# Performance work log

Measured on AMD Instinct MI355X. Metric: run time of the kernel, lower is better.

The kernel has to match this reference:

```python
import jax, jax.numpy as jnp
import numpy as np

WORD_DEPTH, K, K2, L, FL, J = 128, 128, 128, 64, 3, 2


def conv1d(x, w, b):
    # x: [B, C, T], w: [O, I, k], VALID padding (matches nn.Conv1d default)
    y = jax.lax.conv_general_dilated(x, w, (1,), 'VALID',
                                     dimension_numbers=('NCH', 'OIH', 'NCH'))
    return y + b[None, :, None]


def encode(x, w1, b1, w2, b2, ws, bs):
    # x: [B, T, D] -> semantic vector [B, L]
    h = jnp.tanh(conv1d(x.transpose(0, 2, 1), w1, b1))   # [B, K, T-2]
    h = jnp.tanh(conv1d(h, w2, b2))                      # [B, K2, T-4]
    h = h.max(axis=2)                                    # kmax pooling, k=1
    return jnp.tanh(h @ ws.T + bs)                       # [B, L]


def setup_inputs() -> dict:
    key = jax.random.key(0)
    ks = jax.random.split(key, 20)
    B, T = 64, 2048
    s = 0.05
    return {
        'q':    jax.random.normal(ks[0], (B, T, WORD_DEPTH), jnp.float32),
        'pos':  jax.random.normal(ks[1], (B, T, WORD_DEPTH), jnp.float32),
        'negs': jax.random.normal(ks[2], (J, B, T, WORD_DEPTH), jnp.float32),
        'qw1': jax.random.normal(ks[3], (K, WORD_DEPTH, FL), jnp.float32) * s,
        'qb1': jnp.zeros((K,), jnp.float32),
        'qw2': jax.random.normal(ks[4], (K2, K, FL), jnp.float32) * s,
        'qb2': jnp.zeros((K2,), jnp.float32),
        'qsw': jax.random.normal(ks[5], (L, K2), jnp.float32) * s,
        'qsb': jnp.zeros((L,), jnp.float32),
        'dw1': jax.random.normal(ks[6], (K, WORD_DEPTH, FL), jnp.float32) * s,
        'db1': jnp.zeros((K,), jnp.float32),
        'dw2': jax.random.normal(ks[7], (K2, K, FL), jnp.float32) * s,
        'db2': jnp.zeros((K2,), jnp.float32),
        'dsw': jax.random.normal(ks[8], (L, K2), jnp.float32) * s,
        'dsb': jnp.zeros((L,), jnp.float32),
        'gw':  jnp.asarray(1.0, jnp.float32),   # learn_gamma Conv1d(1,1,1) weight
        'gb':  jnp.asarray(0.0, jnp.float32),   # learn_gamma bias
    }


def reference(q, pos, negs, qw1, qb1, qw2, qb2, qsw, qsb,
              dw1, db1, dw2, db2, dsw, dsb, gw, gb):
    Jn, B, T, D = negs.shape
    q_s = encode(q, qw1, qb1, qw2, qb2, qsw, qsb)                  # [B, L]
    pos_s = encode(pos, dw1, db1, dw2, db2, dsw, dsb)              # [B, L]
    neg_s = encode(negs.reshape(Jn * B, T, D),
                   dw1, db1, dw2, db2, dsw, dsb).reshape(Jn, B, L)
    pos_dot = jnp.einsum('bl,bl->b', q_s, pos_s)                   # [B]
    neg_dot = jnp.einsum('bl,jbl->bj', q_s, neg_s)                 # [B, J]
    dots = jnp.concatenate([pos_dot[:, None], neg_dot], axis=1)   # [B, J+1]
    with_gamma = gw * dots + gb                                    # conv1x1
    return jax.nn.softmax(with_gamma, axis=1)                      # [B, J+1]
```

## Files before the change

kernel.cpp:

```cpp
#include <hip/hip_runtime.h>
#include <stdint.h>


typedef __bf16 bf16x8 __attribute__((ext_vector_type(8)));
typedef __bf16 bf16x4 __attribute__((ext_vector_type(4)));
typedef float f32x16 __attribute__((ext_vector_type(16)));
typedef unsigned short u16x8 __attribute__((ext_vector_type(8)));

__device__ __forceinline__ unsigned short f2bf(float f) {
  unsigned u = __builtin_bit_cast(unsigned, f);
  u = u + 0x7FFFu + ((u >> 16) & 1u);
  return (unsigned short)(u >> 16);
}

__device__ __forceinline__ float fast_tanh(float x) {
  x = fminf(10.0f, fmaxf(-10.0f, x));
  float t = __builtin_amdgcn_exp2f(x * -2.8853900817779268f);
  return (1.0f - t) * __builtin_amdgcn_rcpf(1.0f + t);
}

__global__ void prep_kernel(const float* __restrict__ qw1, const float* __restrict__ qw2,
                            const float* __restrict__ dw1, const float* __restrict__ dw2,
                            unsigned short* __restrict__ W1f, unsigned short* __restrict__ W2f) {
  int gid = blockIdx.x * 256 + threadIdx.x;
  int which = gid >= 98304;
  int e = which ? gid - 98304 : gid;
  int br = e / 49152; int r = e % 49152;
  int f = r / 16384; int r2 = r & 16383;
  int kk = r2 >> 11; int row = (r2 >> 4) & 127; int hi = (r2 >> 3) & 1; int j = r2 & 7;
  int c = kk * 16 + hi * 8 + j;
  const float* src = which ? (br ? dw2 : qw2) : (br ? dw1 : qw1);
  (which ? W2f : W1f)[e] = f2bf(src[row * 384 + c * 3 + f]);
}

#define XS0    0
#define H1S0   32768
#define B1_OFF 64512
#define LDS_TOTAL 65024
#define YS 60
#define NWIN 18

__global__ __launch_bounds__(512) void cdssm_main(
    const float* __restrict__ q, const float* __restrict__ pos, const float* __restrict__ negs,
    const unsigned short* __restrict__ W1f, const unsigned short* __restrict__ W2f,
    const float* __restrict__ qb1, const float* __restrict__ db1,
    float* __restrict__ hpart) {
  extern __shared__ char lds[];
  const int tid = threadIdx.x;
  const int bid = blockIdx.x;
  const int seq = bid >> 1;
  const int half = bid & 1;
  const int branch = (seq < 64) ? 0 : 1;
  const float* xptr = (seq < 64) ? (q + (size_t)seq * 2048 * 128)
                    : (seq < 128) ? (pos + (size_t)(seq - 64) * 2048 * 128)
                                  : (negs + (size_t)(seq - 128) * 2048 * 128);
  const float* b1g = branch ? db1 : qb1;
  const int lo = half * 1022;
  const int hi = lo + 1022;

  if (tid < 128) ((float*)(lds + B1_OFF))[tid] = b1g[tid];

  const int lane = tid & 63;
  const int w = tid >> 6;
  const int lrow = lane & 31;
  const int hi5 = lane >> 5;
  const int role = w >> 2;
  const int kt = w & 3;
  const int hi16 = hi5 * 16;

  const unsigned short* wfb = (role ? W2f : W1f) + (size_t)branch * 49152
                              + (kt * 32 + lrow) * 16 + hi5 * 8;

  bf16x8 ap[16];
#pragma unroll
  for (int f = 0; f < 2; ++f)
#pragma unroll
    for (int kk = 0; kk < 8; ++kk)
      ap[f * 8 + kk] = __builtin_bit_cast(bf16x8,
          *(const u16x8*)(wfb + f * 16384 + kk * 2048));

  float vmax[16];
#pragma unroll
  for (int r = 0; r < 16; ++r) vmax[r] = -1e30f;

  const int slot_s = tid >> 4;
  const int d0_s = (tid & 15) * 8;

#pragma unroll
  for (int u = 0; u < 2; ++u) {
    int sl = slot_s + u * 32;
    int t = lo + sl; if (t > 2047) t = 2047;
    const float* src = xptr + ((size_t)t * 128 + d0_s);
    float4 v0 = *(const float4*)src;
    float4 v1 = *(const float4*)(src + 4);
    bf16x8 o;
    o[0] = (__bf16)v0.x; o[1] = (__bf16)v0.y; o[2] = (__bf16)v0.z; o[3] = (__bf16)v0.w;
    o[4] = (__bf16)v1.x; o[5] = (__bf16)v1.y; o[6] = (__bf16)v1.z; o[7] = (__bf16)v1.w;
    *(bf16x8*)(lds + XS0 + sl * 256 + ((d0_s * 2) ^ ((sl & 15) << 4))) = o;
  }
  __syncthreads();

  for (int i = 0; i <= NWIN; ++i) {
    float4 va[4];
    const bool doStage = (i < NWIN - 1);
    if (doStage) {
      const int tb = lo + (i + 1) * YS;
#pragma unroll
      for (int u = 0; u < 2; ++u) {
        int t = tb + slot_s + u * 32; if (t > 2047) t = 2047;
        const float* src = xptr + ((size_t)t * 128 + d0_s);
        va[2 * u]     = *(const float4*)src;
        va[2 * u + 1] = *(const float4*)(src + 4);
      }
    }

    if (role == 0) {
      if (i < NWIN) {
        const int xb = XS0 + (i & 1) * 16384;
        f32x16 acc0, acc1;
#pragma unroll
        for (int r = 0; r < 16; ++r) { acc0[r] = 0.f; acc1[r] = 0.f; }
#pragma unroll
        for (int f = 0; f < 2; ++f) {
          int sv0 = lrow + f;
          int sv1 = 32 + lrow + f; if (sv1 > 63) sv1 = 63;
          int b0 = xb + sv0 * 256, z0 = (sv0 & 15) << 4;
          int b1 = xb + sv1 * 256, z1 = (sv1 & 15) << 4;
#pragma unroll
          for (int kk = 0; kk < 8; ++kk) {
            int ko = kk * 32 + hi16;
            bf16x8 bv0 = __builtin_bit_cast(bf16x8,
                *(const u16x8*)(lds + b0 + (ko ^ z0)));
            acc0 = __builtin_amdgcn_mfma_f32_32x32x16_bf16(ap[f * 8 + kk], bv0, acc0, 0, 0, 0);
            bf16x8 bv1 = __builtin_bit_cast(bf16x8,
                *(const u16x8*)(lds + b1 + (ko ^ z1)));
            acc1 = __builtin_amdgcn_mfma_f32_32x32x16_bf16(ap[f * 8 + kk], bv1, acc1, 0, 0, 0);
          }
        }
        {
          int sv0 = lrow + 2;
          int sv1 = 32 + lrow + 2; if (sv1 > 63) sv1 = 63;
          int b0 = xb + sv0 * 256, z0 = (sv0 & 15) << 4;
          int b1 = xb + sv1 * 256, z1 = (sv1 & 15) << 4;
#pragma unroll
          for (int kk = 0; kk < 8; ++kk) {
            bf16x8 av = __builtin_bit_cast(bf16x8,
                *(const u16x8*)(wfb + 2 * 16384 + kk * 2048));
            int ko = kk * 32 + hi16;
            bf16x8 bv0 = __builtin_bit_cast(bf16x8,
                *(const u16x8*)(lds + b0 + (ko ^ z0)));
            acc0 = __builtin_amdgcn_mfma_f32_32x32x16_bf16(av, bv0, acc0, 0, 0, 0);
            bf16x8 bv1 = __builtin_bit_cast(bf16x8,
                *(const u16x8*)(lds + b1 + (ko ^ z1)));
            acc1 = __builtin_amdgcn_mfma_f32_32x32x16_bf16(av, bv1, acc1, 0, 0, 0);
          }
        }
        const int hb = H1S0 + (i & 1) * 15872;
#pragma unroll
        for (int p = 0; p < 2; ++p) {
          const f32x16 acc = p ? acc1 : acc0;
          int s = p * 32 + lrow;
          if (s < 62) {
            int wb2 = hb + s * 256;
            int wz = (s & 15) << 4;
#pragma unroll
            for (int qd = 0; qd < 4; ++qd) {
              int k0 = kt * 32 + qd * 8 + hi5 * 4;
              float4 bq = *(const float4*)(lds + B1_OFF + k0 * 4);
              bf16x4 hv;
              hv[0] = (__bf16)fast_tanh(acc[qd * 4 + 0] + bq.x);
              hv[1] = (__bf16)fast_tanh(acc[qd * 4 + 1] + bq.y);
              hv[2] = (__bf16)fast_tanh(acc[qd * 4 + 2] + bq.z);
              hv[3] = (__bf16)fast_tanh(acc[qd * 4 + 3] + bq.w);
              *(bf16x4*)(lds + wb2 + ((k0 * 2) ^ wz)) = hv;
            }
          }
        }
      }
    } else {
      if (i >= 1) {
        const int hb = H1S0 + ((i & 1) ^ 1) * 15872;
        f32x16 acc0, acc1;
#pragma unroll
        for (int r = 0; r < 16; ++r) { acc0[r] = 0.f; acc1[r] = 0.f; }
#pragma unroll
        for (int f = 0; f < 2; ++f) {
          int sv0 = lrow + f;
          int sv1 = 32 + lrow + f; if (sv1 > 61) sv1 = 61;
          int b0 = hb + sv0 * 256, z0 = (sv0 & 15) << 4;
          int b1 = hb + sv1 * 256, z1 = (sv1 & 15) << 4;
#pragma unroll
          for (int kk = 0; kk < 8; ++kk) {
            int ko = kk * 32 + hi16;
            bf16x8 bv0 = __builtin_bit_cast(bf16x8,
                *(const u16x8*)(lds + b0 + (ko ^ z0)));
            acc0 = __builtin_amdgcn_mfma_f32_32x32x16_bf16(ap[f * 8 + kk], bv0, acc0, 0, 0, 0);
            bf16x8 bv1 = __builtin_bit_cast(bf16x8,
                *(const u16x8*)(lds + b1 + (ko ^ z1)));
            acc1 = __builtin_amdgcn_mfma_f32_32x32x16_bf16(ap[f * 8 + kk], bv1, acc1, 0, 0, 0);
          }
        }
        {
          int sv0 = lrow + 2;
          int sv1 = 32 + lrow + 2; if (sv1 > 61) sv1 = 61;
          int b0 = hb + sv0 * 256, z0 = (sv0 & 15) << 4;
          int b1 = hb + sv1 * 256, z1 = (sv1 & 15) << 4;
#pragma unroll
          for (int kk = 0; kk < 8; ++kk) {
            bf16x8 av = __builtin_bit_cast(bf16x8,
                *(const u16x8*)(wfb + 2 * 16384 + kk * 2048));
            int ko = kk * 32 + hi16;
            bf16x8 bv0 = __builtin_bit_cast(bf16x8,
                *(const u16x8*)(lds + b0 + (ko ^ z0)));
            acc0 = __builtin_amdgcn_mfma_f32_32x32x16_bf16(av, bv0, acc0, 0, 0, 0);
            bf16x8 bv1 = __builtin_bit_cast(bf16x8,
                *(const u16x8*)(lds + b1 + (ko ^ z1)));
            acc1 = __builtin_amdgcn_mfma_f32_32x32x16_bf16(av, bv1, acc1, 0, 0, 0);
          }
        }
        const int base = lo + (i - 1) * YS;
        const bool valid0 = (base + lrow < hi);
        const int s2b = 32 + lrow;
        const bool valid1 = (s2b < YS) && (base + s2b < hi);
#pragma unroll
        for (int r = 0; r < 16; ++r) {
          float v0 = valid0 ? acc0[r] : -1e30f;
          float v1 = valid1 ? acc1[r] : -1e30f;
          vmax[r] = fmaxf(vmax[r], fmaxf(v0, v1));
        }
      }
    }

    if (doStage) {
      const int xbn = XS0 + ((i + 1) & 1) * 16384;
#pragma unroll
      for (int u = 0; u < 2; ++u) {
        int sl = slot_s + u * 32;
        const float* f0 = (const float*)&va[2 * u];
        bf16x8 o;
#pragma unroll
        for (int j = 0; j < 8; ++j) o[j] = (__bf16)f0[j];
        *(bf16x8*)(lds + xbn + sl * 256 + ((d0_s * 2) ^ ((sl & 15) << 4))) = o;
      }
    }
    __syncthreads();
  }

  if (role == 1) {
#pragma unroll
    for (int r = 0; r < 16; ++r) {
      float v = vmax[r];
      v = fmaxf(v, __shfl_xor(v, 1, 64));
      v = fmaxf(v, __shfl_xor(v, 2, 64));
      v = fmaxf(v, __shfl_xor(v, 4, 64));
      v = fmaxf(v, __shfl_xor(v, 8, 64));
      v = fmaxf(v, __shfl_xor(v, 16, 64));
      vmax[r] = v;
    }
  }
  float* hbuf = (float*)(lds + XS0);
  if (role == 1 && lrow == 0) {
#pragma unroll
    for (int r = 0; r < 16; ++r) {
      int rl = (r & 3) + 8 * (r >> 2) + 4 * hi5;
      hbuf[kt * 32 + rl] = vmax[r];
    }
  }
  __syncthreads();
  if (tid < 128) hpart[(size_t)bid * 128 + tid] = hbuf[tid];
}

__global__ void k2_proj(const float* __restrict__ hpart,
                        const float* __restrict__ qsw, const float* __restrict__ qsb,
                        const float* __restrict__ dsw, const float* __restrict__ dsb,
                        const float* __restrict__ qb2, const float* __restrict__ db2,
                        float* __restrict__ s_out) {
  int seq = blockIdx.x;
  int l = threadIdx.x;
  const float* sw = (seq < 64) ? qsw : dsw;
  const float* sb = (seq < 64) ? qsb : dsb;
  const float* b2 = (seq < 64) ? qb2 : db2;
  const float* h0 = hpart + (size_t)(2 * seq) * 128;
  const float* h1 = h0 + 128;
  float acc = sb[l];
  for (int k = 0; k < 128; ++k)
    acc += fast_tanh(fmaxf(h0[k], h1[k]) + b2[k]) * sw[l * 128 + k];
  s_out[(size_t)seq * 64 + l] = fast_tanh(acc);
}

__global__ void k3_softmax(const float* __restrict__ s_out,
                           const float* __restrict__ gw, const float* __restrict__ gb,
                           float* __restrict__ out) {
  int b = threadIdx.x;
  const float* qs = s_out + (size_t)b * 64;
  const float* ps = s_out + (size_t)(64 + b) * 64;
  const float* n0 = s_out + (size_t)(128 + b) * 64;
  const float* n1 = s_out + (size_t)(192 + b) * 64;
  float d0 = 0.f, d1 = 0.f, d2 = 0.f;
  for (int l = 0; l < 64; ++l) {
    float v = qs[l];
    d0 += v * ps[l];
    d1 += v * n0[l];
    d2 += v * n1[l];
  }
  float g = gw[0], bb = gb[0];
  d0 = g * d0 + bb; d1 = g * d1 + bb; d2 = g * d2 + bb;
  float m = fmaxf(d0, fmaxf(d1, d2));
  float e0 = expf(d0 - m), e1 = expf(d1 - m), e2 = expf(d2 - m);
  float inv = 1.0f / (e0 + e1 + e2);
  out[b * 3 + 0] = e0 * inv;
  out[b * 3 + 1] = e1 * inv;
  out[b * 3 + 2] = e2 * inv;
}

extern "C" void kernel_launch(void* const* d_in, const int* in_sizes, int n_in,
                              void* d_out, int out_size, void* d_ws, size_t ws_size,
                              hipStream_t stream) {
  const float* q    = (const float*)d_in[0];
  const float* pos  = (const float*)d_in[1];
  const float* negs = (const float*)d_in[2];
  const float* qw1  = (const float*)d_in[3];
  const float* qb1  = (const float*)d_in[4];
  const float* qw2  = (const float*)d_in[5];
  const float* qb2  = (const float*)d_in[6];
  const float* qsw  = (const float*)d_in[7];
  const float* qsb  = (const float*)d_in[8];
  const float* dw1  = (const float*)d_in[9];
  const float* db1  = (const float*)d_in[10];
  const float* dw2  = (const float*)d_in[11];
  const float* db2  = (const float*)d_in[12];
  const float* dsw  = (const float*)d_in[13];
  const float* dsb  = (const float*)d_in[14];
  const float* gw   = (const float*)d_in[15];
  const float* gb   = (const float*)d_in[16];
  float* out = (float*)d_out;

  char* ws = (char*)d_ws;
  unsigned short* W1f = (unsigned short*)(ws);
  unsigned short* W2f = (unsigned short*)(ws + 196608);
  float* hpart        = (float*)(ws + 393216);
  float* s_out        = (float*)(ws + 655360);

  hipFuncSetAttribute((const void*)cdssm_main,
                      hipFuncAttributeMaxDynamicSharedMemorySize, LDS_TOTAL);

  prep_kernel<<<768, 256, 0, stream>>>(qw1, qw2, dw1, dw2, W1f, W2f);
  cdssm_main<<<512, 512, LDS_TOTAL, stream>>>(q, pos, negs, W1f, W2f, qb1, db1, hpart);
  k2_proj<<<256, 64, 0, stream>>>(hpart, qsw, qsb, dsw, dsb, qb2, db2, s_out);
  k3_softmax<<<1, 64, 0, stream>>>(s_out, gw, gb, out);
}
```

Measured before the change: 158.6 us.

## Process each sequence in one block instead of splitting time across two

Each workgroup now walks the full 2044-output time axis in 35 windows instead of two workgroups each covering half. This removes the duplicated boundary work and the max-merge of the two partial results in the projection kernel, and halves the partial buffer. It also raises wave priority around the MFMA loops with s_setprio. The cost is half as many workgroups, which reduces per-CU occupancy and the overlap of loads with compute.

New measurement: 135.7 us. 14.4% less time.

```diff
diff --git a/kernel.cpp b/kernel.cpp
--- a/kernel.cpp
+++ b/kernel.cpp
@@ -34,11 +34,14 @@
 }
 
 #define XS0    0
+#define XBUF   16384
 #define H1S0   32768
+#define HBUF   15872
 #define B1_OFF 64512
 #define LDS_TOTAL 65024
 #define YS 60
-#define NWIN 18
+#define NWIN 35
+#define TOUT 2044
 
 __global__ __launch_bounds__(512) void cdssm_main(
     const float* __restrict__ q, const float* __restrict__ pos, const float* __restrict__ negs,
@@ -47,16 +50,12 @@
     float* __restrict__ hpart) {
   extern __shared__ char lds[];
   const int tid = threadIdx.x;
-  const int bid = blockIdx.x;
-  const int seq = bid >> 1;
-  const int half = bid & 1;
+  const int seq = blockIdx.x;
   const int branch = (seq < 64) ? 0 : 1;
   const float* xptr = (seq < 64) ? (q + (size_t)seq * 2048 * 128)
                     : (seq < 128) ? (pos + (size_t)(seq - 64) * 2048 * 128)
                                   : (negs + (size_t)(seq - 128) * 2048 * 128);
   const float* b1g = branch ? db1 : qb1;
-  const int lo = half * 1022;
-  const int hi = lo + 1022;
 
   if (tid < 128) ((float*)(lds + B1_OFF))[tid] = b1g[tid];
 
@@ -89,7 +88,7 @@
 #pragma unroll
   for (int u = 0; u < 2; ++u) {
     int sl = slot_s + u * 32;
-    int t = lo + sl; if (t > 2047) t = 2047;
+    int t = sl;
     const float* src = xptr + ((size_t)t * 128 + d0_s);
     float4 v0 = *(const float4*)src;
     float4 v1 = *(const float4*)(src + 4);
@@ -104,7 +103,7 @@
     float4 va[4];
     const bool doStage = (i < NWIN - 1);
     if (doStage) {
-      const int tb = lo + (i + 1) * YS;
+      const int tb = (i + 1) * YS;
 #pragma unroll
       for (int u = 0; u < 2; ++u) {
         int t = tb + slot_s + u * 32; if (t > 2047) t = 2047;
@@ -116,10 +115,11 @@
 
     if (role == 0) {
       if (i < NWIN) {
-        const int xb = XS0 + (i & 1) * 16384;
+        const int xb = XS0 + (i & 1) * XBUF;
         f32x16 acc0, acc1;
 #pragma unroll
         for (int r = 0; r < 16; ++r) { acc0[r] = 0.f; acc1[r] = 0.f; }
+        __builtin_amdgcn_s_setprio(1);
 #pragma unroll
         for (int f = 0; f < 2; ++f) {
           int sv0 = lrow + f;
@@ -155,7 +155,8 @@
             acc1 = __builtin_amdgcn_mfma_f32_32x32x16_bf16(av, bv1, acc1, 0, 0, 0);
           }
         }
-        const int hb = H1S0 + (i & 1) * 15872;
+        __builtin_amdgcn_s_setprio(0);
+        const int hb = H1S0 + (i & 1) * HBUF;
 #pragma unroll
         for (int p = 0; p < 2; ++p) {
           const f32x16 acc = p ? acc1 : acc0;
@@ -179,10 +180,11 @@
       }
     } else {
       if (i >= 1) {
-        const int hb = H1S0 + ((i & 1) ^ 1) * 15872;
+        const int hb = H1S0 + ((i & 1) ^ 1) * HBUF;
         f32x16 acc0, acc1;
 #pragma unroll
         for (int r = 0; r < 16; ++r) { acc0[r] = 0.f; acc1[r] = 0.f; }
+        __builtin_amdgcn_s_setprio(1);
 #pragma unroll
         for (int f = 0; f < 2; ++f) {
           int sv0 = lrow + f;
@@ -218,10 +220,11 @@
             acc1 = __builtin_amdgcn_mfma_f32_32x32x16_bf16(av, bv1, acc1, 0, 0, 0);
           }
         }
-        const int base = lo + (i - 1) * YS;
-        const bool valid0 = (base + lrow < hi);
+        __builtin_amdgcn_s_setprio(0);
+        const int base = (i - 1) * YS;
+        const bool valid0 = (base + lrow < TOUT);
         const int s2b = 32 + lrow;
-        const bool valid1 = (s2b < YS) && (base + s2b < hi);
+        const bool valid1 = (s2b < YS) && (base + s2b < TOUT);
 #pragma unroll
         for (int r = 0; r < 16; ++r) {
           float v0 = valid0 ? acc0[r] : -1e30f;
@@ -232,7 +235,7 @@
     }
 
     if (doStage) {
-      const int xbn = XS0 + ((i + 1) & 1) * 16384;
+      const int xbn = XS0 + ((i + 1) & 1) * XBUF;
 #pragma unroll
       for (int u = 0; u < 2; ++u) {
         int sl = slot_s + u * 32;
@@ -267,7 +270,7 @@
     }
   }
   __syncthreads();
-  if (tid < 128) hpart[(size_t)bid * 128 + tid] = hbuf[tid];
+  if (tid < 128) hpart[(size_t)seq * 128 + tid] = hbuf[tid];
 }
 
 __global__ void k2_proj(const float* __restrict__ hpart,
@@ -280,11 +283,10 @@
   const float* sw = (seq < 64) ? qsw : dsw;
   const float* sb = (seq < 64) ? qsb : dsb;
   const float* b2 = (seq < 64) ? qb2 : db2;
-  const float* h0 = hpart + (size_t)(2 * seq) * 128;
-  const float* h1 = h0 + 128;
+  const float* h0 = hpart + (size_t)seq * 128;
   float acc = sb[l];
   for (int k = 0; k < 128; ++k)
-    acc += fast_tanh(fmaxf(h0[k], h1[k]) + b2[k]) * sw[l * 128 + k];
+    acc += fast_tanh(h0[k] + b2[k]) * sw[l * 128 + k];
   s_out[(size_t)seq * 64 + l] = fast_tanh(acc);
 }
 
@@ -339,13 +341,13 @@
   unsigned short* W1f = (unsigned short*)(ws);
   unsigned short* W2f = (unsigned short*)(ws + 196608);
   float* hpart        = (float*)(ws + 393216);
-  float* s_out        = (float*)(ws + 655360);
+  float* s_out        = (float*)(ws + 524288);
 
   hipFuncSetAttribute((const void*)cdssm_main,
                       hipFuncAttributeMaxDynamicSharedMemorySize, LDS_TOTAL);
 
   prep_kernel<<<768, 256, 0, stream>>>(qw1, qw2, dw1, dw2, W1f, W2f);
-  cdssm_main<<<512, 512, LDS_TOTAL, stream>>>(q, pos, negs, W1f, W2f, qb1, db1, hpart);
+  cdssm_main<<<256, 512, LDS_TOTAL, stream>>>(q, pos, negs, W1f, W2f, qb1, db1, hpart);
   k2_proj<<<256, 64, 0, stream>>>(hpart, qsw, qsb, dsw, dsb, qb2, db2, s_out);
   k3_softmax<<<1, 64, 0, stream>>>(s_out, gw, gb, out);
 }
```
